# Kernel tuning notes

Measured on AMD Instinct MI355X. Metric: run time of the kernel, lower is better.

## Reference

```python
import jax, jax.numpy as jnp
import numpy as np
from functools import partial

HID = 320
RF = 4
EPS = 1e-5


def lstm_scan(x_seq, Wih, Whh, bih, bhh):
    """PyTorch-style single-layer LSTM. x_seq: [T,B,D] -> outputs [T,B,H]."""
    T, B, _ = x_seq.shape
    H = Whh.shape[1]
    b = bih + bhh  # [4H]
    # precompute input projections for all steps: [T,B,4H]
    xg = jnp.einsum('tbd,gd->tbg', x_seq, Wih) + b

    def step(carry, xg_t):
        h, c = carry
        gates = xg_t + h @ Whh.T  # [B,4H]
        i, f, g, o = jnp.split(gates, 4, axis=-1)  # torch gate order i,f,g,o
        i = jax.nn.sigmoid(i)
        f = jax.nn.sigmoid(f)
        g = jnp.tanh(g)
        o = jax.nn.sigmoid(o)
        c = f * c + i * g
        h = o * jnp.tanh(c)
        return (h, c), h

    h0 = jnp.zeros((B, H), x_seq.dtype)
    (_, _), ys = jax.lax.scan(step, (h0, h0), xg)
    return ys


def conv2d(x, w, b):
    y = jax.lax.conv_general_dilated(x, w, (1, 1), 'VALID',
                                     dimension_numbers=('NCHW', 'OIHW', 'NCHW'))
    return y + b[None, :, None, None]


def maxpool2(x):
    return jax.lax.reduce_window(x, -jnp.inf, jax.lax.max,
                                 (1, 1, 2, 2), (1, 1, 2, 2), 'VALID')


def batchnorm(x, g, b):
    # training-mode BN (batch statistics, biased variance) like nn.BatchNorm2d
    m = x.mean((0, 2, 3), keepdims=True)
    v = x.var((0, 2, 3), keepdims=True)
    return (x - m) * jax.lax.rsqrt(v + EPS) * g[None, :, None, None] + b[None, :, None, None]


def setup_inputs() -> dict:
    key = jax.random.key(0)
    ks = iter(jax.random.split(key, 64))
    s = 0.05
    d = {}
    d['X'] = jax.random.normal(next(ks), (512, 3, 32, 32), jnp.float32)
    d['conv1_w'] = jax.random.normal(next(ks), (128, 3, 3, 3)) * s
    d['conv1_b'] = jnp.zeros((128,))
    d['bn1_g'] = jnp.ones((128,))
    d['bn1_b'] = jnp.zeros((128,))
    d['conv2_w'] = jax.random.normal(next(ks), (48, 128, 4, 4)) * s
    d['conv2_b'] = jnp.zeros((48,))
    d['bn2_g'] = jnp.ones((48,))
    d['bn2_b'] = jnp.zeros((48,))
    for i, din in zip((1, 2, 3, 4), (48, 48, 640, 640)):
        d[f'rnn{i}_Wih'] = jax.random.normal(next(ks), (4 * HID, din)) * s
        d[f'rnn{i}_Whh'] = jax.random.normal(next(ks), (4 * HID, HID)) * s
        d[f'rnn{i}_bih'] = jnp.zeros((4 * HID,))
        d[f'rnn{i}_bhh'] = jnp.zeros((4 * HID,))
    d['dense1_w'] = jax.random.normal(next(ks), (2048, 40960)) * 0.01
    d['dense1_b'] = jnp.zeros((2048,))
    d['dense2_w'] = jax.random.normal(next(ks), (2048, 12 * 12 * 48)) * 0.01
    d['dense2_b'] = jnp.zeros((2048,))
    d['fc_w'] = jax.random.normal(next(ks), (10, 4096)) * 0.01
    d['fc_b'] = jnp.zeros((10,))
    return d


def reference(X, conv1_w, conv1_b, bn1_g, bn1_b, conv2_w, conv2_b, bn2_g, bn2_b,
              rnn1_Wih, rnn1_Whh, rnn1_bih, rnn1_bhh,
              rnn2_Wih, rnn2_Whh, rnn2_bih, rnn2_bhh,
              rnn3_Wih, rnn3_Whh, rnn3_bih, rnn3_bhh,
              rnn4_Wih, rnn4_Whh, rnn4_bih, rnn4_bhh,
              dense1_w, dense1_b, dense2_w, dense2_b, fc_w, fc_b):
    B = X.shape[0]
    ph = pw = 32 // RF  # 8
    # --- fused patch extraction: [B,3,32,32] -> [B,ph,pw,48] (channel-major features) ---
    patches = (X.reshape(B, 3, ph, RF, pw, RF)
                .transpose(0, 2, 4, 1, 3, 5)
                .reshape(B, ph, pw, RF * RF * 3))
    # vertical fw sequence: t = i*pw + j, element = patches[:, j, i, :]
    v_fw = jnp.transpose(patches, (2, 1, 0, 3)).reshape(ph * pw, B, RF * RF * 3)
    v_rev = v_fw[::-1]
    out1 = lstm_scan(v_fw, rnn1_Wih, rnn1_Whh, rnn1_bih, rnn1_bhh)   # [64,B,320]
    out2 = lstm_scan(v_rev, rnn2_Wih, rnn2_Whh, rnn2_bih, rnn2_bhh)
    vfm = jnp.concatenate([out1, out2], axis=2)                       # [64,B,640]
    vfm = vfm.transpose(1, 0, 2).reshape(B, pw, ph, 2 * HID)          # (permute(0,2,1,3) in src is a no-op: not assigned)
    # horizontal sequences are row-major flatten of vfm
    h_fw = vfm.reshape(B, ph * pw, 2 * HID).transpose(1, 0, 2)        # [64,B,640]
    h_rev = h_fw[::-1]
    out3 = lstm_scan(h_fw, rnn3_Wih, rnn3_Whh, rnn3_bih, rnn3_bhh)
    out4 = lstm_scan(h_rev, rnn4_Wih, rnn4_Whh, rnn4_bih, rnn4_bhh)
    hfm = jnp.concatenate([out3, out4], axis=2).transpose(1, 0, 2).reshape(B, ph * pw * 2 * HID)
    output1 = jax.nn.relu(hfm @ dense1_w.T + dense1_b)                # [B,2048]
    # --- LeNet branch ---
    o2 = batchnorm(maxpool2(jax.nn.relu(conv2d(X, conv1_w, conv1_b))), bn1_g, bn1_b)
    o2 = batchnorm(jax.nn.relu(conv2d(o2, conv2_w, conv2_b)), bn2_g, bn2_b)
    o2 = o2.reshape(B, 12 * 12 * 48)
    output2 = jax.nn.relu(o2 @ dense2_w.T + dense2_b)                 # dropout = identity (eval)
    out = jnp.concatenate([output1, output2], axis=1)                 # [B,4096]
    logits = out @ fc_w.T + fc_b
    return jax.nn.log_softmax(logits, axis=-1)
```

## Files before the change

kernel.cpp:

```cpp
#include <hip/hip_runtime.h>
#include <hip/hip_bf16.h>
#include <math.h>

typedef __hip_bfloat16 bf16;
typedef short bf16x8 __attribute__((ext_vector_type(8)));
typedef float f32x4 __attribute__((ext_vector_type(4)));

__device__ __forceinline__ float sigf(float x) { return 1.f / (1.f + expf(-x)); }

template<typename T> __device__ __forceinline__ T cvt_out(float v);
template<> __device__ __forceinline__ float cvt_out<float>(float v) { return v; }
template<> __device__ __forceinline__ bf16  cvt_out<bf16>(float v)  { return __float2bfloat16(v); }

__device__ __forceinline__ unsigned short f2bu(float x) {
  bf16 b = __float2bfloat16(x);
  return *reinterpret_cast<unsigned short*>(&b);
}

__device__ __forceinline__ void load_lds16(const void* g, void* l) {
  __builtin_amdgcn_global_load_lds(
      (const __attribute__((address_space(1))) unsigned int*)g,
      (__attribute__((address_space(3))) unsigned int*)l,
      16, 0, 0);
}

__global__ void patch_kernel(const float* __restrict__ X, float* __restrict__ v) {
  int idx = blockIdx.x * 256 + threadIdx.x;
  int k = idx % 48;
  int b = (idx / 48) % 512;
  int t = idx / (48 * 512);
  int c = k >> 4, r = (k >> 2) & 3, s = k & 3;
  int ph = t & 7, pw = t >> 3;
  v[idx] = X[((b * 3 + c) * 32 + ph * 4 + r) * 32 + pw * 4 + s];
}

__global__ __launch_bounds__(256) void cvt_f32_bf16_k(const float* __restrict__ in,
                                                      bf16* __restrict__ out, size_t n4) {
  size_t i = (size_t)blockIdx.x * 256 + threadIdx.x;
  if (i >= n4) return;
  float4 v = ((const float4*)in)[i];
  ushort4 o;
  o.x = f2bu(v.x); o.y = f2bu(v.y); o.z = f2bu(v.z); o.w = f2bu(v.w);
  ((ushort4*)out)[i] = o;
}

template<typename OutT, bool RELU>
__global__ __launch_bounds__(256) void gemm_nt(
    const float* __restrict__ A, const float* __restrict__ W,
    const float* __restrict__ b1, const float* __restrict__ b2,
    OutT* __restrict__ C, int M, int N, int K, int ldc) {
  __shared__ float As[16][68];
  __shared__ float Ws[16][68];
  int tid = threadIdx.x;
  int tx = tid & 15, ty = tid >> 4;
  int m0 = blockIdx.y << 6, n0 = blockIdx.x << 6;
  const float* Ap = A + (size_t)m0 * K;
  const float* Wp = W + (size_t)n0 * K;
  float acc[4][4] = {};
  for (int k0 = 0; k0 < K; k0 += 16) {
#pragma unroll
    for (int i = 0; i < 4; i++) {
      int idx = tid + (i << 8);
      int row = idx >> 4, col = idx & 15;
      As[col][row] = Ap[(size_t)row * K + k0 + col];
      Ws[col][row] = Wp[(size_t)row * K + k0 + col];
    }
    __syncthreads();
#pragma unroll
    for (int kk = 0; kk < 16; kk++) {
      float4 av = *(const float4*)&As[kk][ty << 2];
      float4 wv = *(const float4*)&Ws[kk][tx << 2];
      float a[4] = {av.x, av.y, av.z, av.w};
      float w[4] = {wv.x, wv.y, wv.z, wv.w};
#pragma unroll
      for (int i = 0; i < 4; i++)
#pragma unroll
        for (int j = 0; j < 4; j++) acc[i][j] += a[i] * w[j];
    }
    __syncthreads();
  }
#pragma unroll
  for (int i = 0; i < 4; i++) {
    int m = m0 + (ty << 2) + i;
#pragma unroll
    for (int j = 0; j < 4; j++) {
      int n = n0 + (tx << 2) + j;
      float v = acc[i][j];
      if (b1) v += b1[n];
      if (b2) v += b2[n];
      if (RELU) v = fmaxf(v, 0.f);
      C[(size_t)m * ldc + n] = cvt_out<OutT>(v);
    }
  }
}

template<typename OutT, bool RELU, bool SPLITK>
__global__ __launch_bounds__(256) void gemm_mfma(
    const bf16* __restrict__ A, const bf16* __restrict__ W,
    const float* __restrict__ b1, const float* __restrict__ b2,
    OutT* __restrict__ C, int M, int N, int K, int ldc, int ksplit) {
  __shared__ __align__(16) short As[128 * 32];
  __shared__ __align__(16) short Ws[128 * 32];
  int tid = threadIdx.x;
  int m0 = blockIdx.y << 7, n0 = blockIdx.x << 7;
  int kb = SPLITK ? blockIdx.z * ksplit : 0;
  int ke = SPLITK ? kb + ksplit : K;
  int w = tid >> 6, lane = tid & 63;
  int wm = (w >> 1) << 6, wn = (w & 1) << 6;
  int lm = lane & 15, quad = lane >> 4;
  f32x4 acc[4][4];
  f32x4 z4 = {0.f, 0.f, 0.f, 0.f};
#pragma unroll
  for (int i = 0; i < 4; i++)
#pragma unroll
    for (int j = 0; j < 4; j++) acc[i][j] = z4;

  int srow = tid >> 2;
  int soff = (tid & 3) * 8;
  const bf16* Ab  = A + (size_t)(m0 + srow) * K + kb + soff;
  const bf16* Ab2 = Ab + (size_t)64 * K;
  const bf16* Wb  = W + (size_t)(n0 + srow) * K + kb + soff;
  const bf16* Wb2 = Wb + (size_t)64 * K;
  short* AL  = &As[(size_t)tid * 8];
  short* AL2 = &As[(size_t)(tid + 256) * 8];
  short* WL  = &Ws[(size_t)tid * 8];
  short* WL2 = &Ws[(size_t)(tid + 256) * 8];

  for (int k0 = kb; k0 < ke; k0 += 32) {
    load_lds16(Ab, AL);  load_lds16(Ab2, AL2);
    load_lds16(Wb, WL);  load_lds16(Wb2, WL2);
    Ab += 32; Ab2 += 32; Wb += 32; Wb2 += 32;
    __syncthreads();
    bf16x8 af[4], wf[4];
#pragma unroll
    for (int i = 0; i < 4; i++) af[i] = *(const bf16x8*)&As[(wm + i * 16 + lm) * 32 + quad * 8];
#pragma unroll
    for (int j = 0; j < 4; j++) wf[j] = *(const bf16x8*)&Ws[(wn + j * 16 + lm) * 32 + quad * 8];
#pragma unroll
    for (int i = 0; i < 4; i++)
#pragma unroll
      for (int j = 0; j < 4; j++)
        acc[i][j] = __builtin_amdgcn_mfma_f32_16x16x32_bf16(af[i], wf[j], acc[i][j], 0, 0, 0);
    __syncthreads();
  }

  if (SPLITK) {
    float* P = (float*)C + (size_t)blockIdx.z * M * N;
#pragma unroll
    for (int i = 0; i < 4; i++)
#pragma unroll
      for (int j = 0; j < 4; j++) {
        int col = n0 + wn + j * 16 + lm;
        int rowb = m0 + wm + i * 16 + quad * 4;
#pragma unroll
        for (int r = 0; r < 4; r++)
          P[(size_t)(rowb + r) * N + col] = acc[i][j][r];
      }
  } else {
#pragma unroll
    for (int i = 0; i < 4; i++)
#pragma unroll
      for (int j = 0; j < 4; j++) {
        int col = n0 + wn + j * 16 + lm;
        int rowb = m0 + wm + i * 16 + quad * 4;
        float bias = (b1 ? b1[col] : 0.f) + (b2 ? b2[col] : 0.f);
#pragma unroll
        for (int r = 0; r < 4; r++) {
          float v = acc[i][j][r] + bias;
          if (RELU) v = fmaxf(v, 0.f);
          C[(size_t)(rowb + r) * ldc + col] = cvt_out<OutT>(v);
        }
      }
  }
}

__global__ __launch_bounds__(256) void splitk_reduce(const float* __restrict__ P,
                                                     const float* __restrict__ bias,
                                                     float* __restrict__ out,
                                                     int MN, int N, int ldc, int nz) {
  int i = blockIdx.x * 256 + threadIdx.x;
  if (i >= MN) return;
  int m = i / N, n = i - m * N;
  float s = bias[n];
  for (int z = 0; z < nz; z++) s += P[(size_t)z * MN + i];
  out[(size_t)m * ldc + n] = fmaxf(s, 0.f);
}

__global__ __launch_bounds__(256) void lstm_step_mfma(
    const bf16* __restrict__ xgF, const bf16* __restrict__ xgR,
    const bf16* __restrict__ WhhA, const bf16* __restrict__ WhhB,
    const bf16* __restrict__ hinA_hi, const bf16* __restrict__ hinA_lo,
    bf16* __restrict__ houtA_hi, bf16* __restrict__ houtA_lo, float* __restrict__ cA,
    const bf16* __restrict__ hinB_hi, const bf16* __restrict__ hinB_lo,
    bf16* __restrict__ houtB_hi, bf16* __restrict__ houtB_lo, float* __restrict__ cB,
    bf16* __restrict__ outA, bf16* __restrict__ outB, int ldo) {
  int lst = blockIdx.z;
  const bf16* xg  = lst ? xgR : xgF;
  const bf16* Whh = lst ? WhhB : WhhA;
  const bf16* hhi = lst ? hinB_hi : hinA_hi;
  const bf16* hlo = lst ? hinB_lo : hinA_lo;
  bf16* hohi = lst ? houtB_hi : houtA_hi;
  bf16* holo = lst ? houtB_lo : houtA_lo;
  float* c   = lst ? cB : cA;
  bf16* out  = lst ? outB : outA;
  int j0 = blockIdx.x << 5;
  int r0 = blockIdx.y << 6;

  __shared__ __align__(16) short Ah[64 * 32];
  __shared__ __align__(16) short Al[64 * 32];
  __shared__ __align__(16) short Bs[128 * 32];
  __shared__ float G[64 * 129];

  int tid = threadIdx.x;
  int g = tid >> 6, lane = tid & 63;
  int lm = lane & 15, quad = lane >> 4;
  f32x4 acc[4][2];
  f32x4 z4 = {0.f, 0.f, 0.f, 0.f};
#pragma unroll
  for (int i = 0; i < 4; i++) { acc[i][0] = z4; acc[i][1] = z4; }

  int srow = tid >> 2;
  int soff = (tid & 3) * 8;
  const bf16* Ahb = hhi + (size_t)(r0 + srow) * 320 + soff;
  const bf16* Alb = hlo + (size_t)(r0 + srow) * 320 + soff;
  int br1 = tid >> 2;
  int br2 = br1 + 64;
  int grow1 = (br1 >> 5) * 320 + j0 + (br1 & 31);
  int grow2 = (br2 >> 5) * 320 + j0 + (br2 & 31);
  const bf16* Bb1 = Whh + (size_t)grow1 * 320 + soff;
  const bf16* Bb2 = Whh + (size_t)grow2 * 320 + soff;
  short* AhL = &Ah[(size_t)tid * 8];
  short* AlL = &Al[(size_t)tid * 8];
  short* BL1 = &Bs[(size_t)tid * 8];
  short* BL2 = &Bs[(size_t)(tid + 256) * 8];

  for (int k0 = 0; k0 < 320; k0 += 32) {
    load_lds16(Ahb, AhL); load_lds16(Alb, AlL);
    load_lds16(Bb1, BL1); load_lds16(Bb2, BL2);
    Ahb += 32; Alb += 32; Bb1 += 32; Bb2 += 32;
    __syncthreads();
    bf16x8 ah[4], alv[4], bv[2];
#pragma unroll
    for (int i = 0; i < 4; i++) {
      ah[i]  = *(const bf16x8*)&Ah[(i * 16 + lm) * 32 + quad * 8];
      alv[i] = *(const bf16x8*)&Al[(i * 16 + lm) * 32 + quad * 8];
    }
#pragma unroll
    for (int j = 0; j < 2; j++) bv[j] = *(const bf16x8*)&Bs[(g * 32 + j * 16 + lm) * 32 + quad * 8];
#pragma unroll
    for (int i = 0; i < 4; i++)
#pragma unroll
      for (int j = 0; j < 2; j++) {
        acc[i][j] = __builtin_amdgcn_mfma_f32_16x16x32_bf16(ah[i],  bv[j], acc[i][j], 0, 0, 0);
        acc[i][j] = __builtin_amdgcn_mfma_f32_16x16x32_bf16(alv[i], bv[j], acc[i][j], 0, 0, 0);
      }
    __syncthreads();
  }

#pragma unroll
  for (int i = 0; i < 4; i++)
#pragma unroll
    for (int j = 0; j < 2; j++)
#pragma unroll
      for (int r = 0; r < 4; r++)
        G[(i * 16 + quad * 4 + r) * 129 + g * 32 + j * 16 + lm] = acc[i][j][r];
  __syncthreads();

  int rl = tid >> 2;
  int jb = (tid & 3) * 8;
  int r = r0 + rl;
#pragma unroll
  for (int q = 0; q < 8; q++) {
    int jl = jb + q;
    int jh = j0 + jl;
    float pre[4];
#pragma unroll
    for (int g2 = 0; g2 < 4; g2++)
      pre[g2] = G[rl * 129 + g2 * 32 + jl] +
                __bfloat162float(xg[(size_t)r * 1280 + g2 * 320 + jh]);
    float iv = sigf(pre[0]), fv = sigf(pre[1]), gv = tanhf(pre[2]), ov = sigf(pre[3]);
    size_t sb = (size_t)r * 320 + jh;
    float cn = fv * c[sb] + iv * gv;
    float hn = ov * tanhf(cn);
    c[sb] = cn;
    bf16 hb = __float2bfloat16(hn);
    hohi[sb] = hb;
    holo[sb] = __float2bfloat16(hn - __bfloat162float(hb));
    out[(size_t)r * ldo + jh] = hb;
  }
}

__global__ __launch_bounds__(256) void conv1_pool(
    const float* __restrict__ X, const float* __restrict__ w,
    const float* __restrict__ bias, float* __restrict__ pool) {
  int b = blockIdx.x;
  __shared__ float Xs[3 * 32 * 32];
  __shared__ float Wl[128 * 27];
  __shared__ float Bl[128];
  int tid = threadIdx.x;
  for (int i = tid; i < 3072; i += 256) Xs[i] = X[(size_t)b * 3072 + i];
  for (int i = tid; i < 3456; i += 256) Wl[i] = w[i];
  if (tid < 128) Bl[tid] = bias[tid];
  __syncthreads();
  int oc = tid & 127, half = tid >> 7;
  float wr[27];
#pragma unroll
  for (int q = 0; q < 27; q++) wr[q] = Wl[oc * 27 + q];
  float bv = Bl[oc];
  for (int p = half; p < 225; p += 2) {
    int i = p / 15, j = p % 15;
    float mx = -3.4e38f;
#pragma unroll
    for (int dy = 0; dy < 2; dy++)
#pragma unroll
      for (int dx = 0; dx < 2; dx++) {
        float s = bv;
        int rb = 2 * i + dy, cb = 2 * j + dx;
#pragma unroll
        for (int cc = 0; cc < 3; cc++)
#pragma unroll
          for (int kr = 0; kr < 3; kr++)
#pragma unroll
            for (int kc = 0; kc < 3; kc++)
              s += wr[cc * 9 + kr * 3 + kc] * Xs[cc * 1024 + (rb + kr) * 32 + cb + kc];
        mx = fmaxf(mx, s);
      }
    pool[((size_t)(b * 128 + oc)) * 225 + p] = fmaxf(mx, 0.f);
  }
}

__global__ void bn_stats(const float* __restrict__ x, int C, int per, int B,
                         const float* __restrict__ g, const float* __restrict__ bb,
                         float* __restrict__ a, float* __restrict__ s) {
  int c = blockIdx.x;
  int n = B * per;
  float sum = 0.f, sq = 0.f;
  for (int i = threadIdx.x; i < n; i += 256) {
    int b = i / per, p = i - b * per;
    float v = x[((size_t)b * C + c) * per + p];
    sum += v; sq += v * v;
  }
  __shared__ float S1[256], S2[256];
  S1[threadIdx.x] = sum; S2[threadIdx.x] = sq;
  __syncthreads();
  for (int off = 128; off > 0; off >>= 1) {
    if (threadIdx.x < off) { S1[threadIdx.x] += S1[threadIdx.x + off]; S2[threadIdx.x] += S2[threadIdx.x + off]; }
    __syncthreads();
  }
  if (threadIdx.x == 0) {
    float m = S1[0] / n;
    float var = S2[0] / n - m * m;
    float av = g[c] * rsqrtf(var + 1e-5f);
    a[c] = av; s[c] = bb[c] - m * av;
  }
}

__global__ void bn_apply_bf16(const float* __restrict__ x, bf16* __restrict__ y,
                              const float* __restrict__ a, const float* __restrict__ s,
                              int per, int C, size_t total) {
  size_t i = (size_t)blockIdx.x * 256 + threadIdx.x;
  if (i < total) {
    int ch = (int)((i / per) % C);
    y[i] = __float2bfloat16(a[ch] * x[i] + s[ch]);
  }
}

__global__ __launch_bounds__(192) void conv2_kernel(
    const float* __restrict__ pool, const float* __restrict__ w,
    const float* __restrict__ bias, const float* __restrict__ a1,
    const float* __restrict__ s1, float* __restrict__ out) {
  int rg = blockIdx.x, b = blockIdx.y;
  int r0 = rg * 4;
  __shared__ float L[128 * 7 * 15];
  int tid = threadIdx.x;
#pragma unroll
  for (int i = 0; i < 70; i++) {
    int idx = tid + i * 192;
    int c = idx / 105, rem = idx % 105;
    int r = rem / 15, col = rem % 15;
    L[idx] = pool[((size_t)(b * 128 + c)) * 225 + (r0 + r) * 15 + col] * a1[c] + s1[c];
  }
  __syncthreads();
  int oc = tid % 48, orow = tid / 48;
  float acc[12];
  float bv = bias[oc];
#pragma unroll
  for (int j = 0; j < 12; j++) acc[j] = bv;
  for (int c = 0; c < 128; c++) {
#pragma unroll
    for (int kr = 0; kr < 4; kr++) {
      float v[15];
#pragma unroll
      for (int q = 0; q < 15; q++) v[q] = L[(c * 7 + orow + kr) * 15 + q];
      const float* wp = &w[((size_t)(oc * 128 + c)) * 16 + kr * 4];
#pragma unroll
      for (int kc = 0; kc < 4; kc++) {
        float wv = wp[kc];
#pragma unroll
        for (int j = 0; j < 12; j++) acc[j] += wv * v[j + kc];
      }
    }
  }
  float* op = &out[((size_t)(b * 48 + oc)) * 144 + (r0 + orow) * 12];
#pragma unroll
  for (int j = 0; j < 12; j++) op[j] = fmaxf(acc[j], 0.f);
}

__global__ __launch_bounds__(64) void fc_logsoftmax(
    const float* __restrict__ A, const float* __restrict__ W,
    const float* __restrict__ bias, float* __restrict__ out) {
  int b = blockIdx.x, lane = threadIdx.x;
  float acc[10] = {};
  for (int k = lane; k < 4096; k += 64) {
    float x = A[(size_t)b * 4096 + k];
#pragma unroll
    for (int o = 0; o < 10; o++) acc[o] += x * W[o * 4096 + k];
  }
#pragma unroll
  for (int o = 0; o < 10; o++)
    for (int off = 32; off > 0; off >>= 1) acc[o] += __shfl_down(acc[o], off);
  if (lane == 0) {
    float l[10];
    float m = -3.4e38f;
#pragma unroll
    for (int o = 0; o < 10; o++) { l[o] = acc[o] + bias[o]; m = fmaxf(m, l[o]); }
    float se = 0.f;
#pragma unroll
    for (int o = 0; o < 10; o++) se += expf(l[o] - m);
    float ls = logf(se);
#pragma unroll
    for (int o = 0; o < 10; o++) out[b * 10 + o] = l[o] - m - ls;
  }
}

__global__ void zero_k(float* __restrict__ p, size_t n) {
  size_t i = (size_t)blockIdx.x * 256 + threadIdx.x;
  if (i < n) p[i] = 0.f;
}

extern "C" void kernel_launch(void* const* d_in, const int* in_sizes, int n_in,
                              void* d_out, int out_size, void* d_ws, size_t ws_size,
                              hipStream_t stream) {
  const float* X    = (const float*)d_in[0];
  const float* c1w  = (const float*)d_in[1];
  const float* c1b  = (const float*)d_in[2];
  const float* bn1g = (const float*)d_in[3];
  const float* bn1b = (const float*)d_in[4];
  const float* c2w  = (const float*)d_in[5];
  const float* c2b  = (const float*)d_in[6];
  const float* bn2g = (const float*)d_in[7];
  const float* bn2b = (const float*)d_in[8];
  const float *Wih[4], *Whh[4], *bih[4], *bhh[4];
  for (int i = 0; i < 4; i++) {
    Wih[i] = (const float*)d_in[9 + 4 * i];
    Whh[i] = (const float*)d_in[10 + 4 * i];
    bih[i] = (const float*)d_in[11 + 4 * i];
    bhh[i] = (const float*)d_in[12 + 4 * i];
  }
  const float* d1w = (const float*)d_in[25];
  const float* d1b = (const float*)d_in[26];
  const float* d2w = (const float*)d_in[27];
  const float* d2b = (const float*)d_in[28];
  const float* fcw = (const float*)d_in[29];
  const float* fcb = (const float*)d_in[30];
  float* out = (float*)d_out;

  char* p = (char*)d_ws;
  float* v_fw = (float*)p;  p += (size_t)64 * 512 * 48 * 4;
  char* R = p;              p += (size_t)167772160;
  bf16* xgA = (bf16*)R;
  bf16* xgB = xgA + (size_t)41943040;
  bf16* h_fw = (bf16*)p;    p += (size_t)64 * 512 * 640 * 2;
  bf16* hfm  = (bf16*)p;    p += (size_t)512 * 40960 * 2;
  bf16* wih3b = (bf16*)p;   p += (size_t)1280 * 640 * 2;
  bf16* wih4b = (bf16*)p;   p += (size_t)1280 * 640 * 2;
  bf16* whhb[4];
  for (int i = 0; i < 4; i++) { whhb[i] = (bf16*)p; p += (size_t)1280 * 320 * 2; }
  float* states = (float*)p; p += (size_t)3932160;
  float* P = (float*)p;      p += (size_t)4 * 512 * 2048 * 4;
  float* outcat = (float*)p; p += (size_t)512 * 4096 * 4;
  float* bnp = (float*)p;    p += 2048;
  float* pool   = (float*)R;
  float* c2out  = (float*)(R + 58982400);
  bf16*  c2outb = (bf16*)(R + 58982400 + 14155776);
  bf16*  d2wb   = (bf16*)(R + 58982400 + 14155776 + 7077888);
  bf16*  d1wb   = (bf16*)R;
  float* a1 = bnp, *s1 = bnp + 128, *a2 = bnp + 256, *s2 = bnp + 304;

  float* cA = states;
  float* cB = cA + 163840;
  bf16* hb = (bf16*)(cB + 163840);
  bf16* hA0h = hb;             bf16* hA0l = hb + 163840;
  bf16* hA1h = hb + 327680;    bf16* hA1l = hb + 491520;
  bf16* hB0h = hb + 655360;    bf16* hB0l = hb + 819200;
  bf16* hB1h = hb + 983040;    bf16* hB1l = hb + 1146880;

  patch_kernel<<<6144, 256, 0, stream>>>(X, v_fw);
  for (int i = 0; i < 4; i++)
    cvt_f32_bf16_k<<<400, 256, 0, stream>>>(Whh[i], whhb[i], 102400);
  cvt_f32_bf16_k<<<800, 256, 0, stream>>>(Wih[2], wih3b, 204800);
  cvt_f32_bf16_k<<<800, 256, 0, stream>>>(Wih[3], wih4b, 204800);

  gemm_nt<bf16, false><<<dim3(20, 512), 256, 0, stream>>>(v_fw, Wih[0], bih[0], bhh[0], xgA, 32768, 1280, 48, 1280);
  gemm_nt<bf16, false><<<dim3(20, 512), 256, 0, stream>>>(v_fw, Wih[1], bih[1], bhh[1], xgB, 32768, 1280, 48, 1280);

  zero_k<<<3840, 256, 0, stream>>>(states, (size_t)983040);
  for (int t = 0; t < 64; t++) {
    const bf16* xf = xgA + (size_t)t * 655360;
    const bf16* xr = xgB + (size_t)(63 - t) * 655360;
    bf16* oA = h_fw + (size_t)t * 327680;
    if (t & 1)
      lstm_step_mfma<<<dim3(10, 8, 2), 256, 0, stream>>>(xf, xr, whhb[0], whhb[1],
          hA1h, hA1l, hA0h, hA0l, cA, hB1h, hB1l, hB0h, hB0l, cB, oA, oA + 320, 640);
    else
      lstm_step_mfma<<<dim3(10, 8, 2), 256, 0, stream>>>(xf, xr, whhb[0], whhb[1],
          hA0h, hA0l, hA1h, hA1l, cA, hB0h, hB0l, hB1h, hB1l, cB, oA, oA + 320, 640);
  }

  gemm_mfma<bf16, false, false><<<dim3(10, 256, 1), 256, 0, stream>>>(h_fw, wih3b, bih[2], bhh[2], xgA, 32768, 1280, 640, 1280, 0);
  gemm_mfma<bf16, false, false><<<dim3(10, 256, 1), 256, 0, stream>>>(h_fw, wih4b, bih[3], bhh[3], xgB, 32768, 1280, 640, 1280, 0);

  zero_k<<<3840, 256, 0, stream>>>(states, (size_t)983040);
  for (int t = 0; t < 64; t++) {
    const bf16* xf = xgA + (size_t)t * 655360;
    const bf16* xr = xgB + (size_t)(63 - t) * 655360;
    bf16* oA = hfm + (size_t)t * 640;
    if (t & 1)
      lstm_step_mfma<<<dim3(10, 8, 2), 256, 0, stream>>>(xf, xr, whhb[2], whhb[3],
          hA1h, hA1l, hA0h, hA0l, cA, hB1h, hB1l, hB0h, hB0l, cB, oA, oA + 320, 40960);
    else
      lstm_step_mfma<<<dim3(10, 8, 2), 256, 0, stream>>>(xf, xr, whhb[2], whhb[3],
          hA0h, hA0l, hA1h, hA1l, cA, hB0h, hB0l, hB1h, hB1l, cB, oA, oA + 320, 40960);
  }

  cvt_f32_bf16_k<<<81920, 256, 0, stream>>>(d1w, d1wb, 20971520);
  gemm_mfma<float, false, true><<<dim3(16, 4, 4), 256, 0, stream>>>(hfm, d1wb, nullptr, nullptr, P, 512, 2048, 40960, 2048, 10240);
  splitk_reduce<<<4096, 256, 0, stream>>>(P, d1b, outcat, 1048576, 2048, 4096, 4);

  conv1_pool<<<512, 256, 0, stream>>>(X, c1w, c1b, pool);
  bn_stats<<<128, 256, 0, stream>>>(pool, 128, 225, 512, bn1g, bn1b, a1, s1);
  conv2_kernel<<<dim3(3, 512), 192, 0, stream>>>(pool, c2w, c2b, a1, s1, c2out);
  bn_stats<<<48, 256, 0, stream>>>(c2out, 48, 144, 512, bn2g, bn2b, a2, s2);
  bn_apply_bf16<<<13824, 256, 0, stream>>>(c2out, c2outb, a2, s2, 144, 48, (size_t)3538944);

  cvt_f32_bf16_k<<<13824, 256, 0, stream>>>(d2w, d2wb, 3538944);
  gemm_mfma<float, false, true><<<dim3(16, 4, 4), 256, 0, stream>>>(c2outb, d2wb, nullptr, nullptr, P, 512, 2048, 6912, 2048, 1728);
  splitk_reduce<<<4096, 256, 0, stream>>>(P, d2b, outcat + 2048, 1048576, 2048, 4096, 4);

  fc_logsoftmax<<<512, 64, 0, stream>>>(outcat, fcw, fcb, out);
}
```

Before: 3.961 ms.

## Replace per-step LSTM launches with persistent kernel using grid barrier

The 64 per-timestep launches per bidirectional LSTM pair are replaced by one persistent kernel of 160 blocks. Each block keeps its slice of Whh resident in swizzled LDS and holds the cell state in registers, and a global atomic barrier separates timesteps. This removes launch overhead, the repeated Whh reloads and the global c-state traffic, and it vectorises the xg and h loads and stores. In exchange it relies on all 160 blocks being co-resident for the spin barrier, and it uses 120KB of LDS per block, which limits occupancy to one block per CU.

```diff
diff --git a/kernel.cpp b/kernel.cpp
--- a/kernel.cpp
+++ b/kernel.cpp
@@ -186,107 +186,148 @@
   out[(size_t)m * ldc + n] = fmaxf(s, 0.f);
 }
 
-__global__ __launch_bounds__(256) void lstm_step_mfma(
-    const bf16* __restrict__ xgF, const bf16* __restrict__ xgR,
+__global__ __launch_bounds__(256) void lstm_scan_persist(
+    const bf16* __restrict__ xgA_, const bf16* __restrict__ xgB_,
     const bf16* __restrict__ WhhA, const bf16* __restrict__ WhhB,
-    const bf16* __restrict__ hinA_hi, const bf16* __restrict__ hinA_lo,
-    bf16* __restrict__ houtA_hi, bf16* __restrict__ houtA_lo, float* __restrict__ cA,
-    const bf16* __restrict__ hinB_hi, const bf16* __restrict__ hinB_lo,
-    bf16* __restrict__ houtB_hi, bf16* __restrict__ houtB_lo, float* __restrict__ cB,
-    bf16* __restrict__ outA, bf16* __restrict__ outB, int ldo) {
-  int lst = blockIdx.z;
-  const bf16* xg  = lst ? xgR : xgF;
+    bf16* hAhi0, bf16* hAlo0, bf16* hAhi1, bf16* hAlo1,
+    bf16* hBhi0, bf16* hBlo0, bf16* hBhi1, bf16* hBlo1,
+    bf16* __restrict__ outb, long long tstride, int ldo,
+    unsigned* bar_cnt, unsigned* bar_gen) {
+  constexpr unsigned TOTAL = 160;
+  __shared__ __align__(16) char smem[122880];
+  short* WsS = (short*)smem;
+  short* AhS = (short*)(smem + 81920);
+  short* AlS = (short*)(smem + 102400);
+  float* G   = (float*)(smem + 81920);
+
+  const int tid = threadIdx.x;
+  const int jt = blockIdx.x, rt = blockIdx.y, lst = blockIdx.z;
+  const int j0 = jt << 5, r0 = rt << 6;
   const bf16* Whh = lst ? WhhB : WhhA;
-  const bf16* hhi = lst ? hinB_hi : hinA_hi;
-  const bf16* hlo = lst ? hinB_lo : hinA_lo;
-  bf16* hohi = lst ? houtB_hi : houtA_hi;
-  bf16* holo = lst ? houtB_lo : houtA_lo;
-  float* c   = lst ? cB : cA;
-  bf16* out  = lst ? outB : outA;
-  int j0 = blockIdx.x << 5;
-  int r0 = blockIdx.y << 6;
-
-  __shared__ __align__(16) short Ah[64 * 32];
-  __shared__ __align__(16) short Al[64 * 32];
-  __shared__ __align__(16) short Bs[128 * 32];
-  __shared__ float G[64 * 129];
-
-  int tid = threadIdx.x;
-  int g = tid >> 6, lane = tid & 63;
-  int lm = lane & 15, quad = lane >> 4;
-  f32x4 acc[4][2];
-  f32x4 z4 = {0.f, 0.f, 0.f, 0.f};
-#pragma unroll
-  for (int i = 0; i < 4; i++) { acc[i][0] = z4; acc[i][1] = z4; }
-
-  int srow = tid >> 2;
-  int soff = (tid & 3) * 8;
-  const bf16* Ahb = hhi + (size_t)(r0 + srow) * 320 + soff;
-  const bf16* Alb = hlo + (size_t)(r0 + srow) * 320 + soff;
-  int br1 = tid >> 2;
-  int br2 = br1 + 64;
-  int grow1 = (br1 >> 5) * 320 + j0 + (br1 & 31);
-  int grow2 = (br2 >> 5) * 320 + j0 + (br2 & 31);
-  const bf16* Bb1 = Whh + (size_t)grow1 * 320 + soff;
-  const bf16* Bb2 = Whh + (size_t)grow2 * 320 + soff;
-  short* AhL = &Ah[(size_t)tid * 8];
-  short* AlL = &Al[(size_t)tid * 8];
-  short* BL1 = &Bs[(size_t)tid * 8];
-  short* BL2 = &Bs[(size_t)(tid + 256) * 8];
-
-  for (int k0 = 0; k0 < 320; k0 += 32) {
-    load_lds16(Ahb, AhL); load_lds16(Alb, AlL);
-    load_lds16(Bb1, BL1); load_lds16(Bb2, BL2);
-    Ahb += 32; Alb += 32; Bb1 += 32; Bb2 += 32;
+  const bf16* xg0 = lst ? xgB_ : xgA_;
+  bf16* hhi[2] = { lst ? hBhi0 : hAhi0, lst ? hBhi1 : hAhi1 };
+  bf16* hlo[2] = { lst ? hBlo0 : hAlo0, lst ? hBlo1 : hAlo1 };
+
+  for (int i = 0; i < 20; i++) {
+    int idx = i * 256 + tid;
+    int row = idx / 40, pc = idx - row * 40;
+    int gk = pc ^ (row & 7);
+    int grow = ((row >> 5) * 320) + j0 + (row & 31);
+    load_lds16(Whh + (size_t)grow * 320 + gk * 8, (char*)WsS + (size_t)idx * 16);
+  }
+  __syncthreads();
+
+  const int g = tid >> 6, lane = tid & 63;
+  const int lm = lane & 15, quad = lane >> 4;
+  const int srow = tid >> 2, skoff = (tid & 3) * 8;
+  const int rl = tid >> 2, jb = (tid & 3) * 8;
+  const int r = r0 + rl;
+
+  float cs[8];
+#pragma unroll
+  for (int q = 0; q < 8; q++) cs[q] = 0.f;
+
+  for (int t = 0; t < 64; t++) {
+    const bf16* xg = xg0 + (size_t)(lst ? 63 - t : t) * 655360;
+    int par = t & 1;
+    const bf16* hi_in = hhi[par];
+    const bf16* lo_in = hlo[par];
+    bf16* hi_out = hhi[par ^ 1];
+    bf16* lo_out = hlo[par ^ 1];
+
+    f32x4 acc[4][2];
+    f32x4 z4 = {0.f, 0.f, 0.f, 0.f};
+#pragma unroll
+    for (int i = 0; i < 4; i++) { acc[i][0] = z4; acc[i][1] = z4; }
+
+    if (t > 0) {
+      const bf16* hb = hi_in + (size_t)(r0 + srow) * 320 + skoff;
+      const bf16* lb = lo_in + (size_t)(r0 + srow) * 320 + skoff;
+#pragma unroll
+      for (int half = 0; half < 2; half++) {
+#pragma unroll
+        for (int ci = 0; ci < 5; ci++) {
+          load_lds16(hb + half * 160 + ci * 32, (char*)AhS + ci * 4096 + (size_t)tid * 16);
+          load_lds16(lb + half * 160 + ci * 32, (char*)AlS + ci * 4096 + (size_t)tid * 16);
+        }
+        __syncthreads();
+#pragma unroll
+        for (int ci = 0; ci < 5; ci++) {
+          bf16x8 ah[4], al[4], bv[2];
+          const short* Ab = AhS + ci * 2048;
+          const short* Al2 = AlS + ci * 2048;
+#pragma unroll
+          for (int i = 0; i < 4; i++) {
+            ah[i] = *(const bf16x8*)&Ab[(i * 16 + lm) * 32 + quad * 8];
+            al[i] = *(const bf16x8*)&Al2[(i * 16 + lm) * 32 + quad * 8];
+          }
+          int kc8 = half * 20 + ci * 4 + quad;
+#pragma unroll
+          for (int j = 0; j < 2; j++) {
+            int nrow = g * 32 + j * 16 + lm;
+            bv[j] = *(const bf16x8*)&WsS[nrow * 320 + ((kc8 ^ (nrow & 7)) << 3)];
+          }
+#pragma unroll
+          for (int i = 0; i < 4; i++)
+#pragma unroll
+            for (int j = 0; j < 2; j++) {
+              acc[i][j] = __builtin_amdgcn_mfma_f32_16x16x32_bf16(ah[i], bv[j], acc[i][j], 0, 0, 0);
+              acc[i][j] = __builtin_amdgcn_mfma_f32_16x16x32_bf16(al[i], bv[j], acc[i][j], 0, 0, 0);
+            }
+        }
+        __syncthreads();
+      }
+    }
+
+#pragma unroll
+    for (int i = 0; i < 4; i++)
+#pragma unroll
+      for (int j = 0; j < 2; j++)
+#pragma unroll
+        for (int rr = 0; rr < 4; rr++)
+          G[(i * 16 + quad * 4 + rr) * 129 + g * 32 + j * 16 + lm] = acc[i][j][rr];
     __syncthreads();
-    bf16x8 ah[4], alv[4], bv[2];
-#pragma unroll
-    for (int i = 0; i < 4; i++) {
-      ah[i]  = *(const bf16x8*)&Ah[(i * 16 + lm) * 32 + quad * 8];
-      alv[i] = *(const bf16x8*)&Al[(i * 16 + lm) * 32 + quad * 8];
-    }
-#pragma unroll
-    for (int j = 0; j < 2; j++) bv[j] = *(const bf16x8*)&Bs[(g * 32 + j * 16 + lm) * 32 + quad * 8];
-#pragma unroll
-    for (int i = 0; i < 4; i++)
-#pragma unroll
-      for (int j = 0; j < 2; j++) {
-        acc[i][j] = __builtin_amdgcn_mfma_f32_16x16x32_bf16(ah[i],  bv[j], acc[i][j], 0, 0, 0);
-        acc[i][j] = __builtin_amdgcn_mfma_f32_16x16x32_bf16(alv[i], bv[j], acc[i][j], 0, 0, 0);
+
+    union { bf16x8 v; bf16 b[8]; } xv0, xv1, xv2, xv3, hv, lv;
+    xv0.v = *(const bf16x8*)&xg[(size_t)r * 1280 + 0 * 320 + j0 + jb];
+    xv1.v = *(const bf16x8*)&xg[(size_t)r * 1280 + 1 * 320 + j0 + jb];
+    xv2.v = *(const bf16x8*)&xg[(size_t)r * 1280 + 2 * 320 + j0 + jb];
+    xv3.v = *(const bf16x8*)&xg[(size_t)r * 1280 + 3 * 320 + j0 + jb];
+#pragma unroll
+    for (int q = 0; q < 8; q++) {
+      float p0 = G[rl * 129 + 0 * 32 + jb + q] + __bfloat162float(xv0.b[q]);
+      float p1 = G[rl * 129 + 1 * 32 + jb + q] + __bfloat162float(xv1.b[q]);
+      float p2 = G[rl * 129 + 2 * 32 + jb + q] + __bfloat162float(xv2.b[q]);
+      float p3 = G[rl * 129 + 3 * 32 + jb + q] + __bfloat162float(xv3.b[q]);
+      float iv = sigf(p0), fv = sigf(p1), gv = tanhf(p2), ov = sigf(p3);
+      float cn = fv * cs[q] + iv * gv;
+      cs[q] = cn;
+      float hn = ov * tanhf(cn);
+      hv.b[q] = __float2bfloat16(hn);
+      lv.b[q] = __float2bfloat16(hn - __bfloat162float(hv.b[q]));
+    }
+    size_t hoff = (size_t)r * 320 + j0 + jb;
+    *(bf16x8*)(hi_out + hoff) = hv.v;
+    *(bf16x8*)(lo_out + hoff) = lv.v;
+    *(bf16x8*)(outb + (size_t)t * tstride + (size_t)r * ldo + lst * 320 + j0 + jb) = hv.v;
+
+    if (t < 63) {
+      __threadfence();
+      __syncthreads();
+      if (tid == 0) {
+        unsigned g0 = __hip_atomic_load(bar_gen, __ATOMIC_RELAXED, __HIP_MEMORY_SCOPE_AGENT);
+        unsigned old = __hip_atomic_fetch_add(bar_cnt, 1u, __ATOMIC_ACQ_REL, __HIP_MEMORY_SCOPE_AGENT);
+        if (old == TOTAL - 1u) {
+          __hip_atomic_store(bar_cnt, 0u, __ATOMIC_RELAXED, __HIP_MEMORY_SCOPE_AGENT);
+          __hip_atomic_fetch_add(bar_gen, 1u, __ATOMIC_ACQ_REL, __HIP_MEMORY_SCOPE_AGENT);
+        } else {
+          while (__hip_atomic_load(bar_gen, __ATOMIC_RELAXED, __HIP_MEMORY_SCOPE_AGENT) == g0)
+            __builtin_amdgcn_s_sleep(1);
+        }
       }
-    __syncthreads();
-  }
-
-#pragma unroll
-  for (int i = 0; i < 4; i++)
-#pragma unroll
-    for (int j = 0; j < 2; j++)
-#pragma unroll
-      for (int r = 0; r < 4; r++)
-        G[(i * 16 + quad * 4 + r) * 129 + g * 32 + j * 16 + lm] = acc[i][j][r];
-  __syncthreads();
-
-  int rl = tid >> 2;
-  int jb = (tid & 3) * 8;
-  int r = r0 + rl;
-#pragma unroll
-  for (int q = 0; q < 8; q++) {
-    int jl = jb + q;
-    int jh = j0 + jl;
-    float pre[4];
-#pragma unroll
-    for (int g2 = 0; g2 < 4; g2++)
-      pre[g2] = G[rl * 129 + g2 * 32 + jl] +
-                __bfloat162float(xg[(size_t)r * 1280 + g2 * 320 + jh]);
-    float iv = sigf(pre[0]), fv = sigf(pre[1]), gv = tanhf(pre[2]), ov = sigf(pre[3]);
-    size_t sb = (size_t)r * 320 + jh;
-    float cn = fv * c[sb] + iv * gv;
-    float hn = ov * tanhf(cn);
-    c[sb] = cn;
-    bf16 hb = __float2bfloat16(hn);
-    hohi[sb] = hb;
-    holo[sb] = __float2bfloat16(hn - __bfloat162float(hb));
-    out[(size_t)r * ldo + jh] = hb;
+      __syncthreads();
+      __threadfence();
+    }
   }
 }
 
@@ -476,10 +517,11 @@
   bf16* wih4b = (bf16*)p;   p += (size_t)1280 * 640 * 2;
   bf16* whhb[4];
   for (int i = 0; i < 4; i++) { whhb[i] = (bf16*)p; p += (size_t)1280 * 320 * 2; }
-  float* states = (float*)p; p += (size_t)3932160;
+  bf16* hstates = (bf16*)p;  p += (size_t)8 * 163840 * 2;
   float* P = (float*)p;      p += (size_t)4 * 512 * 2048 * 4;
   float* outcat = (float*)p; p += (size_t)512 * 4096 * 4;
   float* bnp = (float*)p;    p += 2048;
+  unsigned* bar = (unsigned*)p; p += 256;
   float* pool   = (float*)R;
   float* c2out  = (float*)(R + 58982400);
   bf16*  c2outb = (bf16*)(R + 58982400 + 14155776);
@@ -487,51 +529,35 @@
   bf16*  d1wb   = (bf16*)R;
   float* a1 = bnp, *s1 = bnp + 128, *a2 = bnp + 256, *s2 = bnp + 304;
 
-  float* cA = states;
-  float* cB = cA + 163840;
-  bf16* hb = (bf16*)(cB + 163840);
-  bf16* hA0h = hb;             bf16* hA0l = hb + 163840;
-  bf16* hA1h = hb + 327680;    bf16* hA1l = hb + 491520;
-  bf16* hB0h = hb + 655360;    bf16* hB0l = hb + 819200;
-  bf16* hB1h = hb + 983040;    bf16* hB1l = hb + 1146880;
+  bf16* hA0h = hstates;
+  bf16* hA0l = hstates + 163840;
+  bf16* hA1h = hstates + 327680;
+  bf16* hA1l = hstates + 491520;
+  bf16* hB0h = hstates + 655360;
+  bf16* hB0l = hstates + 819200;
+  bf16* hB1h = hstates + 983040;
+  bf16* hB1l = hstates + 1146880;
 
   patch_kernel<<<6144, 256, 0, stream>>>(X, v_fw);
   for (int i = 0; i < 4; i++)
     cvt_f32_bf16_k<<<400, 256, 0, stream>>>(Whh[i], whhb[i], 102400);
   cvt_f32_bf16_k<<<800, 256, 0, stream>>>(Wih[2], wih3b, 204800);
   cvt_f32_bf16_k<<<800, 256, 0, stream>>>(Wih[3], wih4b, 204800);
+  zero_k<<<1, 64, 0, stream>>>((float*)bar, 64);
 
   gemm_nt<bf16, false><<<dim3(20, 512), 256, 0, stream>>>(v_fw, Wih[0], bih[0], bhh[0], xgA, 32768, 1280, 48, 1280);
   gemm_nt<bf16, false><<<dim3(20, 512), 256, 0, stream>>>(v_fw, Wih[1], bih[1], bhh[1], xgB, 32768, 1280, 48, 1280);
 
-  zero_k<<<3840, 256, 0, stream>>>(states, (size_t)983040);
-  for (int t = 0; t < 64; t++) {
-    const bf16* xf = xgA + (size_t)t * 655360;
-    const bf16* xr = xgB + (size_t)(63 - t) * 655360;
-    bf16* oA = h_fw + (size_t)t * 327680;
-    if (t & 1)
-      lstm_step_mfma<<<dim3(10, 8, 2), 256, 0, stream>>>(xf, xr, whhb[0], whhb[1],
-          hA1h, hA1l, hA0h, hA0l, cA, hB1h, hB1l, hB0h, hB0l, cB, oA, oA + 320, 640);
-    else
-      lstm_step_mfma<<<dim3(10, 8, 2), 256, 0, stream>>>(xf, xr, whhb[0], whhb[1],
-          hA0h, hA0l, hA1h, hA1l, cA, hB0h, hB0l, hB1h, hB1l, cB, oA, oA + 320, 640);
-  }
+  lstm_scan_persist<<<dim3(10, 8, 2), 256, 0, stream>>>(xgA, xgB, whhb[0], whhb[1],
+      hA0h, hA0l, hA1h, hA1l, hB0h, hB0l, hB1h, hB1l,
+      h_fw, 327680LL, 640, bar, bar + 16);
 
   gemm_mfma<bf16, false, false><<<dim3(10, 256, 1), 256, 0, stream>>>(h_fw, wih3b, bih[2], bhh[2], xgA, 32768, 1280, 640, 1280, 0);
   gemm_mfma<bf16, false, false><<<dim3(10, 256, 1), 256, 0, stream>>>(h_fw, wih4b, bih[3], bhh[3], xgB, 32768, 1280, 640, 1280, 0);
 
-  zero_k<<<3840, 256, 0, stream>>>(states, (size_t)983040);
-  for (int t = 0; t < 64; t++) {
-    const bf16* xf = xgA + (size_t)t * 655360;
-    const bf16* xr = xgB + (size_t)(63 - t) * 655360;
-    bf16* oA = hfm + (size_t)t * 640;
-    if (t & 1)
-      lstm_step_mfma<<<dim3(10, 8, 2), 256, 0, stream>>>(xf, xr, whhb[2], whhb[3],
-          hA1h, hA1l, hA0h, hA0l, cA, hB1h, hB1l, hB0h, hB0l, cB, oA, oA + 320, 40960);
-    else
-      lstm_step_mfma<<<dim3(10, 8, 2), 256, 0, stream>>>(xf, xr, whhb[2], whhb[3],
-          hA0h, hA0l, hA1h, hA1l, cA, hB0h, hB0l, hB1h, hB1l, cB, oA, oA + 320, 40960);
-  }
+  lstm_scan_persist<<<dim3(10, 8, 2), 256, 0, stream>>>(xgA, xgB, whhb[2], whhb[3],
+      hA0h, hA0l, hA1h, hA1l, hB0h, hB0l, hB1h, hB1l,
+      hfm, 640LL, 40960, bar, bar + 16);
 
   cvt_f32_bf16_k<<<81920, 256, 0, stream>>>(d1w, d1wb, 20971520);
   gemm_mfma<float, false, true><<<dim3(16, 4, 4), 256, 0, stream>>>(hfm, d1wb, nullptr, nullptr, P, 512, 2048, 40960, 2048, 10240);
```

Measured after the change: 8.481 ms. 114% more time.
